# Performance work log

Measured on AMD Instinct MI355X. Metric: run time of the kernel, lower is better.

The kernel has to match this reference:

```python
import jax, jax.numpy as jnp
import numpy as np

NUM_HEADS = 8
NUM_GROUPS = 32
EPS = 1e-5


def group_norm(x, gamma, beta):
    b, c, h, w = x.shape
    xg = x.reshape(b, NUM_GROUPS, c // NUM_GROUPS, h, w)
    mean = jnp.mean(xg, axis=(2, 3, 4), keepdims=True)
    var = jnp.var(xg, axis=(2, 3, 4), keepdims=True)
    xn = ((xg - mean) * jax.lax.rsqrt(var + EPS)).reshape(b, c, h, w)
    return xn * gamma[None, :, None, None] + beta[None, :, None, None]


def setup_inputs() -> dict:
    key = jax.random.key(0)
    ks = jax.random.split(key, 4)
    b, c, h, w = 16, 512, 32, 32
    x = jax.random.normal(ks[0], (b, c, h, w), dtype=jnp.float32)
    gn_gamma = jnp.ones((c,), dtype=jnp.float32)
    gn_beta = jnp.zeros((c,), dtype=jnp.float32)
    qkv_w = jax.random.normal(ks[1], (3 * c, c), dtype=jnp.float32) * (1.0 / np.sqrt(c))
    qkv_b = jnp.zeros((3 * c,), dtype=jnp.float32)
    proj_w = jax.random.normal(ks[2], (c, c), dtype=jnp.float32) * (1.0 / np.sqrt(c))
    proj_b = jnp.zeros((c,), dtype=jnp.float32)
    return {"x": x, "gn_gamma": gn_gamma, "gn_beta": gn_beta,
            "qkv_w": qkv_w, "qkv_b": qkv_b, "proj_w": proj_w, "proj_b": proj_b}


def reference(x, gn_gamma, gn_beta, qkv_w, qkv_b, proj_w, proj_b):
    b, c, h, w = x.shape
    hd = c // NUM_HEADS
    hw = h * w

    xn = group_norm(x, gn_gamma, gn_beta)
    # 1x1 conv == channel matmul
    qkv = jnp.einsum('oc,bchw->bohw', qkv_w, xn) + qkv_b[None, :, None, None]
    q, k, v = jnp.split(qkv, 3, axis=1)
    q = q.reshape(b, NUM_HEADS, hd, hw)
    k = k.reshape(b, NUM_HEADS, hd, hw)
    v = v.reshape(b, NUM_HEADS, hd, hw)

    scale = 1.0 / np.sqrt(hd)
    attn = jnp.einsum('bhdt,bhds->bhts', q, k) * scale  # [b,H,hw,hw]
    attn = jax.nn.softmax(attn, axis=-1)
    h_attn = jnp.einsum('bhts,bhds->bhdt', attn, v).reshape(b, c, h, w)

    h_attn = jnp.einsum('oc,bchw->bohw', proj_w, h_attn) + proj_b[None, :, None, None]
    return x + h_attn
```

## Files before the change

### kernel.cpp

```cpp
#include <hip/hip_runtime.h>
#include <math.h>

#define NUM_HEADS 8
#define NUM_GROUPS 32
#define EPS 1e-5f

constexpr int B  = 16;
constexpr int C  = 512;
constexpr int HW = 1024;
constexpr int HD = 64;

typedef short bf16x8 __attribute__((ext_vector_type(8)));
typedef float f32x4  __attribute__((ext_vector_type(4)));

#define QSCALE 0.1803368801111f

__device__ inline unsigned short f2bf(float f) {
    union { float f; unsigned int u; } v; v.f = f;
    unsigned int r = (v.u + 0x7FFFu + ((v.u >> 16) & 1u)) >> 16;
    return (unsigned short)r;
}

__device__ __forceinline__ unsigned int pack_trunc(float lo, float hi) {
    return __builtin_amdgcn_perm(__float_as_uint(hi), __float_as_uint(lo), 0x07060302u);
}

__device__ __forceinline__ float exp2_raw(float x) {
#if __has_builtin(__builtin_amdgcn_exp2f)
    return __builtin_amdgcn_exp2f(x);
#else
    float r; asm("v_exp_f32 %0, %1" : "=v"(r) : "v"(x)); return r;
#endif
}

__device__ __forceinline__ void gld_lds16(void* lds, const void* g) {
    __builtin_amdgcn_global_load_lds(
        (const __attribute__((address_space(1))) void*)g,
        (__attribute__((address_space(3))) void*)lds, 16, 0, 0);
}

__device__ __forceinline__ void pl32_swap(unsigned int& a, unsigned int& b) {
#if __has_builtin(__builtin_amdgcn_permlane32_swap)
    auto r = __builtin_amdgcn_permlane32_swap(a, b, false, false);
    a = r[0]; b = r[1];
#else
    asm volatile("v_permlane32_swap_b32 %0, %1" : "+v"(a), "+v"(b));
#endif
}
__device__ __forceinline__ void pl16_swap(unsigned int& a, unsigned int& b) {
#if __has_builtin(__builtin_amdgcn_permlane16_swap)
    auto r = __builtin_amdgcn_permlane16_swap(a, b, false, false);
    a = r[0]; b = r[1];
#else
    asm volatile("v_permlane16_swap_b32 %0, %1" : "+v"(a), "+v"(b));
#endif
}

#define ABAR(VM) do {                                                   \
    asm volatile("s_waitcnt vmcnt(" VM ")\n\ts_barrier" ::: "memory");  \
    __builtin_amdgcn_sched_barrier(0);                                  \
} while (0)

__global__ __launch_bounds__(256)
void groupnorm_t_kernel(const float* __restrict__ x,
                        const float* __restrict__ gamma,
                        const float* __restrict__ beta,
                        unsigned short* __restrict__ xnT) {
    const int bg = blockIdx.x;
    const int b = bg >> 5, g = bg & 31;
    const size_t base = ((size_t)b * C + (size_t)g * 16) * HW;

    float v[4][16];
    float sum = 0.f, sumsq = 0.f;
    #pragma unroll
    for (int p = 0; p < 4; ++p) {
        const int t = threadIdx.x + p * 256;
        #pragma unroll
        for (int cl = 0; cl < 16; ++cl) {
            const float f = x[base + (size_t)cl * HW + t];
            v[p][cl] = f;
            sum += f;
            sumsq += f * f;
        }
    }
    #pragma unroll
    for (int off = 32; off > 0; off >>= 1) {
        sum   += __shfl_down(sum, off, 64);
        sumsq += __shfl_down(sumsq, off, 64);
    }
    __shared__ float s_sum[4], s_sq[4];
    const int wid = threadIdx.x >> 6, lane = threadIdx.x & 63;
    if (lane == 0) { s_sum[wid] = sum; s_sq[wid] = sumsq; }
    __syncthreads();
    const float tsum = s_sum[0] + s_sum[1] + s_sum[2] + s_sum[3];
    const float tsq  = s_sq[0] + s_sq[1] + s_sq[2] + s_sq[3];
    const float mean = tsum * (1.0f / 16384.f);
    const float var  = tsq * (1.0f / 16384.f) - mean * mean;
    const float rstd = rsqrtf(var + EPS);

    float ga[16], be[16];
    #pragma unroll
    for (int cl = 0; cl < 16; ++cl) {
        ga[cl] = gamma[g * 16 + cl] * rstd;
        be[cl] = beta[g * 16 + cl] - mean * ga[cl];
    }

    #pragma unroll
    for (int p = 0; p < 4; ++p) {
        const int t = threadIdx.x + p * 256;
        unsigned short pk[16];
        #pragma unroll
        for (int cl = 0; cl < 16; ++cl)
            pk[cl] = f2bf(v[p][cl] * ga[cl] + be[cl]);
        unsigned short* dst = xnT + ((size_t)(b * 1024 + t)) * 512 + g * 16;
        *(uint4*)dst = *(const uint4*)pk;
        *(uint4*)(dst + 8) = *(const uint4*)(pk + 8);
    }
}

__global__ __launch_bounds__(256)
void wconv_kernel(const float* __restrict__ qkv_w,
                  const float* __restrict__ proj_w,
                  unsigned short* __restrict__ wqb) {
    const int i = blockIdx.x * 256 + threadIdx.x;
    const int n1 = 786432 / 4;
    const int nt = 1048576 / 4;
    if (i >= nt) return;
    const float4 v = (i < n1) ? ((const float4*)qkv_w)[i]
                              : ((const float4*)proj_w)[i - n1];
    ushort4 r;
    r.x = f2bf(v.x); r.y = f2bf(v.y); r.z = f2bf(v.z); r.w = f2bf(v.w);
    ((ushort4*)wqb)[i] = r;
}

__device__ __forceinline__ void mfma_gemm_core(const char* __restrict__ Ab,
                                               const char* __restrict__ Bb,
                                               unsigned short* As,
                                               unsigned short* Bs,
                                               f32x4 acc[4][4]) {
    const int tid = threadIdx.x;
    const int w = tid >> 6, lane = tid & 63;
    const int lo = lane & 15, q4 = lane >> 4;
    const int wm = w >> 1, wn = w & 1;
    const int lrow = lane >> 2, lkc = lane & 3;

    for (int k0 = 0; k0 < 512; k0 += 32) {
        __syncthreads();
        #pragma unroll
        for (int i = 0; i < 2; ++i) {
            const int row = w * 32 + i * 16 + lrow;
            const int kc = lkc ^ ((row >> 1) & 3);
            const size_t goff = (size_t)row * 1024 + k0 * 2 + kc * 16;
            gld_lds16((char*)As + w * 2048 + i * 1024, Ab + goff);
            gld_lds16((char*)Bs + w * 2048 + i * 1024, Bb + goff);
        }
        __syncthreads();

        bf16x8 af[4], bfr[4];
        #pragma unroll
        for (int i = 0; i < 4; ++i) {
            const int ra = wm * 64 + i * 16 + lo;
            af[i]  = *(const bf16x8*)(As + ra * 32 + (q4 ^ ((ra >> 1) & 3)) * 8);
            const int rb = wn * 64 + i * 16 + lo;
            bfr[i] = *(const bf16x8*)(Bs + rb * 32 + (q4 ^ ((rb >> 1) & 3)) * 8);
        }
        #pragma unroll
        for (int mi = 0; mi < 4; ++mi)
            #pragma unroll
            for (int ni = 0; ni < 4; ++ni)
                acc[mi][ni] = __builtin_amdgcn_mfma_f32_16x16x32_bf16(
                    af[mi], bfr[ni], acc[mi][ni], 0, 0, 0);
    }
}

__global__ __launch_bounds__(256)
void qkv_mfma_kernel(const unsigned short* __restrict__ wqb,
                     const unsigned short* __restrict__ xnT,
                     const float* __restrict__ qkv_b,
                     unsigned short* __restrict__ Qt,
                     unsigned short* __restrict__ Kt,
                     unsigned short* __restrict__ Vb) {
    __shared__ __align__(16) unsigned short SMEM[8192];
    unsigned short* As = SMEM;
    unsigned short* Bs = SMEM + 4096;
    const int batch = blockIdx.z;
    const int mBase = blockIdx.y * 128, nBase = blockIdx.x * 128;

    f32x4 acc[4][4] = {};
    mfma_gemm_core((const char*)(wqb + (size_t)mBase * 512),
                   (const char*)(xnT + ((size_t)batch * 1024 + nBase) * 512),
                   As, Bs, acc);

    const int tid = threadIdx.x;
    const int w = tid >> 6, lane = tid & 63;
    const int lo = lane & 15, q4 = lane >> 4;
    const int wm = w >> 1, wn = w & 1;
    const int mw = mBase + wm * 64;
    const int tb = nBase + wn * 64;

    __syncthreads();

    if (mw < 1024) {
        const bool isQ = mw < 512;
        const int head = (mw >> 6) & 7;
        unsigned short* dst = (isQ ? Qt : Kt) + (((size_t)batch * 8 + head) << 16);
        const float sc = isQ ? QSCALE : 1.0f;
        #pragma unroll
        for (int mi = 0; mi < 4; ++mi) {
            const float4 bq = *(const float4*)(qkv_b + mw + mi * 16 + q4 * 4);
            #pragma unroll
            for (int ni = 0; ni < 4; ++ni) {
                const int t = tb + ni * 16 + lo;
                ushort4 pk;
                pk.x = f2bf((acc[mi][ni][0] + bq.x) * sc);
                pk.y = f2bf((acc[mi][ni][1] + bq.y) * sc);
                pk.z = f2bf((acc[mi][ni][2] + bq.z) * sc);
                pk.w = f2bf((acc[mi][ni][3] + bq.w) * sc);
                *(ushort4*)(dst + (size_t)t * 64 + mi * 16 + q4 * 4) = pk;
            }
        }
    } else {
        unsigned short* T = SMEM + w * 2048;
        unsigned short* Vrow = Vb + (size_t)batch * 524288 + (size_t)(mw - 1024) * 1024 + tb;
        const int rl8 = lane >> 3, c8 = lane & 7;
        #pragma unroll
        for (int p = 0; p < 2; ++p) {
            #pragma unroll
            for (int mi2 = 0; mi2 < 2; ++mi2) {
                const int mi = 2 * p + mi2;
                const float4 bq = *(const float4*)(qkv_b + mw + mi * 16 + q4 * 4);
                const int dl = mi2 * 16 + q4 * 4;
                #pragma unroll
                for (int ni = 0; ni < 4; ++ni) {
                    const int tl = ni * 16 + lo;
                    T[(dl + 0) * 64 + tl] = f2bf(acc[mi][ni][0] + bq.x);
                    T[(dl + 1) * 64 + tl] = f2bf(acc[mi][ni][1] + bq.y);
                    T[(dl + 2) * 64 + tl] = f2bf(acc[mi][ni][2] + bq.z);
                    T[(dl + 3) * 64 + tl] = f2bf(acc[mi][ni][3] + bq.w);
                }
            }
            #pragma unroll
            for (int i = 0; i < 4; ++i) {
                const int dl = i * 8 + rl8;
                const uint4 val = *(const uint4*)&T[dl * 64 + c8 * 8];
                *(uint4*)(Vrow + (size_t)(p * 32 + dl) * 1024 + c8 * 8) = val;
            }
        }
    }
}

__device__ __forceinline__ void attn_stage(const unsigned short* __restrict__ Kp,
                                           const unsigned short* __restrict__ Vp,
                                           int s0, unsigned short* Kd,
                                           unsigned short* Vd,
                                           int w, int rl, int p8) {
    #pragma unroll
    for (int cc = 0; cc < 2; ++cc) {
        const int r = 16 * w + 8 * cc + rl;
        const int jj = p8 ^ (r & 7);
        gld_lds16(Kd + (16 * w + 8 * cc) * 64, Kp + (size_t)(s0 + r) * 64 + jj * 8);
        gld_lds16(Vd + (16 * w + 8 * cc) * 64, Vp + (size_t)r * 1024 + s0 + jj * 8);
    }
}

__device__ __forceinline__ void attn_chunk(const unsigned short* __restrict__ Kc,
                                           const unsigned short* __restrict__ Vc,
                                           const bf16x8 (&qf)[2][2],
                                           f32x4 (&oacc)[4][2], float (&lrun)[2],
                                           int lo, int q4, int xr) {
    f32x4 sacc[4][2] = {};
    __builtin_amdgcn_s_setprio(1);
    #pragma unroll
    for (int mt = 0; mt < 4; ++mt) {
        const unsigned short* kr = Kc + (16 * mt + lo) * 64;
        const bf16x8 a0 = *(const bf16x8*)(kr + ((q4    ) ^ xr) * 8);
        const bf16x8 a1 = *(const bf16x8*)(kr + ((q4 + 4) ^ xr) * 8);
        #pragma unroll
        for (int nt = 0; nt < 2; ++nt) {
            sacc[mt][nt] = __builtin_amdgcn_mfma_f32_16x16x32_bf16(a0, qf[nt][0], sacc[mt][nt], 0, 0, 0);
            sacc[mt][nt] = __builtin_amdgcn_mfma_f32_16x16x32_bf16(a1, qf[nt][1], sacc[mt][nt], 0, 0, 0);
        }
    }
    __builtin_amdgcn_s_setprio(0);

    bf16x8 bp[2][2];
    #pragma unroll
    for (int nt = 0; nt < 2; ++nt) {
        unsigned int X[4][2];
        float ps = 0.f;
        #pragma unroll
        for (int mt = 0; mt < 4; ++mt) {
            const f32x4 s = sacc[mt][nt];
            const float p0 = exp2_raw(s[0]);
            const float p1 = exp2_raw(s[1]);
            const float p2 = exp2_raw(s[2]);
            const float p3 = exp2_raw(s[3]);
            ps += (p0 + p1) + (p2 + p3);
            X[mt][0] = pack_trunc(p0, p1);
            X[mt][1] = pack_trunc(p2, p3);
        }
        lrun[nt] += ps;
        #pragma unroll
        for (int h2 = 0; h2 < 2; ++h2) {
            unsigned int Y0, Y1, Y2, Y3;
            {
                unsigned int a = X[2 * h2][0], bb = X[2 * h2 + 1][0];
                pl32_swap(a, bb);
                pl16_swap(a, bb);
                Y0 = a; Y2 = bb;
            }
            {
                unsigned int a = X[2 * h2][1], bb = X[2 * h2 + 1][1];
                pl32_swap(a, bb);
                pl16_swap(a, bb);
                Y1 = a; Y3 = bb;
            }
            union { unsigned int u[4]; bf16x8 v; } cv;
            cv.u[0] = Y0; cv.u[1] = Y1; cv.u[2] = Y2; cv.u[3] = Y3;
            bp[nt][h2] = cv.v;
        }
    }

    __builtin_amdgcn_s_setprio(1);
    #pragma unroll
    for (int md = 0; md < 4; ++md) {
        const unsigned short* vr = Vc + (16 * md + lo) * 64;
        const bf16x8 v0 = *(const bf16x8*)(vr + ((q4    ) ^ xr) * 8);
        const bf16x8 v1 = *(const bf16x8*)(vr + ((q4 + 4) ^ xr) * 8);
        #pragma unroll
        for (int nt = 0; nt < 2; ++nt) {
            oacc[md][nt] = __builtin_amdgcn_mfma_f32_16x16x32_bf16(v0, bp[nt][0], oacc[md][nt], 0, 0, 0);
            oacc[md][nt] = __builtin_amdgcn_mfma_f32_16x16x32_bf16(v1, bp[nt][1], oacc[md][nt], 0, 0, 0);
        }
    }
    __builtin_amdgcn_s_setprio(0);
}

__global__ __launch_bounds__(256, 3)
void attn_mfma_kernel(const unsigned short* __restrict__ Qt,
                      const unsigned short* __restrict__ Kt,
                      const unsigned short* __restrict__ Vb,
                      unsigned short* __restrict__ attnT) {
    const int bh = blockIdx.x;
    const int b = bh >> 3, h = bh & 7;
    const int tBase = blockIdx.y * 128;
    const int tid = threadIdx.x;
    const int w = tid >> 6, lane = tid & 63;
    const int lo = lane & 15, q4 = lane >> 4;
    const int xr = lo & 7;

    __shared__ __align__(16) unsigned short Ks[3][64 * 64];
    __shared__ __align__(16) unsigned short Vs[3][64 * 64];

    const unsigned short* Kp = Kt + ((size_t)bh << 16);
    const unsigned short* Vp = Vb + ((size_t)b * 512 + h * 64) * 1024;

    bf16x8 qf[2][2];
    {
        const unsigned short* Qp = Qt + ((size_t)bh * 1024 + tBase + 32 * w) * 64;
        #pragma unroll
        for (int nt = 0; nt < 2; ++nt) {
            qf[nt][0] = *(const bf16x8*)(Qp + (size_t)(16 * nt + lo) * 64 + 8 * q4);
            qf[nt][1] = *(const bf16x8*)(Qp + (size_t)(16 * nt + lo) * 64 + 32 + 8 * q4);
        }
    }

    const int rl = lane >> 3, p8 = lane & 7;

    f32x4 oacc[4][2] = {};
    float lrun[2] = {0.f, 0.f};

    attn_stage(Kp, Vp, 0 * 64, Ks[0], Vs[0], w, rl, p8);
    attn_stage(Kp, Vp, 1 * 64, Ks[1], Vs[1], w, rl, p8);

    ABAR("4");
    attn_stage(Kp, Vp, 2 * 64, Ks[2], Vs[2], w, rl, p8);
    attn_chunk(Ks[0], Vs[0], qf, oacc, lrun, lo, q4, xr);

    #pragma unroll 1
    for (int ii = 0; ii < 4; ++ii) {
        const int i = 3 * ii + 1;
        ABAR("4");
        attn_stage(Kp, Vp, (i + 2) * 64, Ks[0], Vs[0], w, rl, p8);
        attn_chunk(Ks[1], Vs[1], qf, oacc, lrun, lo, q4, xr);
        ABAR("4");
        attn_stage(Kp, Vp, (i + 3) * 64, Ks[1], Vs[1], w, rl, p8);
        attn_chunk(Ks[2], Vs[2], qf, oacc, lrun, lo, q4, xr);
        ABAR("4");
        attn_stage(Kp, Vp, (i + 4) * 64, Ks[2], Vs[2], w, rl, p8);
        attn_chunk(Ks[0], Vs[0], qf, oacc, lrun, lo, q4, xr);
    }

    ABAR("4");
    attn_stage(Kp, Vp, 15 * 64, Ks[0], Vs[0], w, rl, p8);
    attn_chunk(Ks[1], Vs[1], qf, oacc, lrun, lo, q4, xr);
    ABAR("4");
    attn_chunk(Ks[2], Vs[2], qf, oacc, lrun, lo, q4, xr);
    ABAR("0");
    attn_chunk(Ks[0], Vs[0], qf, oacc, lrun, lo, q4, xr);

    #pragma unroll
    for (int nt = 0; nt < 2; ++nt) {
        float lt = lrun[nt];
        lt += __shfl_xor(lt, 16, 64);
        lt += __shfl_xor(lt, 32, 64);
        const float inv = 1.0f / lt;
        const int t = tBase + 32 * w + 16 * nt + lo;
        unsigned short* op = attnT + ((size_t)(b * 1024 + t)) * 512 + h * 64;
        #pragma unroll
        for (int md = 0; md < 4; ++md) {
            uint2 pk;
            pk.x = pack_trunc(oacc[md][nt][0] * inv, oacc[md][nt][1] * inv);
            pk.y = pack_trunc(oacc[md][nt][2] * inv, oacc[md][nt][3] * inv);
            *(uint2*)(op + 16 * md + 4 * q4) = pk;
        }
    }
}

__global__ __launch_bounds__(256)
void proj_mfma_kernel(const unsigned short* __restrict__ wpb,
                      const unsigned short* __restrict__ attnT,
                      const float* __restrict__ proj_b,
                      const float* __restrict__ x,
                      float* __restrict__ out) {
    __shared__ __align__(16) unsigned short As[128 * 32];
    __shared__ __align__(16) unsigned short Bs[128 * 32];
    const int batch = blockIdx.z;
    const int mBase = blockIdx.y * 128, nBase = blockIdx.x * 128;

    f32x4 acc[4][4] = {};
    mfma_gemm_core((const char*)(wpb + (size_t)mBase * 512),
                   (const char*)(attnT + ((size_t)batch * 1024 + nBase) * 512),
                   As, Bs, acc);

    const int tid = threadIdx.x;
    const int w = tid >> 6, lane = tid & 63;
    const int lo = lane & 15, q4 = lane >> 4;
    const int wm = w >> 1, wn = w & 1;
    const float* xb = x + (size_t)batch * 524288;
    float* ob = out + (size_t)batch * 524288;

    #pragma unroll
    for (int mi = 0; mi < 4; ++mi) {
        const int m0 = mBase + wm * 64 + mi * 16 + q4 * 4;
        const float4 bq = *(const float4*)(proj_b + m0);
        #pragma unroll
        for (int ni = 0; ni < 4; ++ni) {
            const int t = nBase + wn * 64 + ni * 16 + lo;
            const size_t o0 = (size_t)m0 * 1024 + t;
            ob[o0]          = acc[mi][ni][0] + bq.x + xb[o0];
            ob[o0 + 1024]   = acc[mi][ni][1] + bq.y + xb[o0 + 1024];
            ob[o0 + 2048]   = acc[mi][ni][2] + bq.z + xb[o0 + 2048];
            ob[o0 + 3072]   = acc[mi][ni][3] + bq.w + xb[o0 + 3072];
        }
    }
}

extern "C" void kernel_launch(void* const* d_in, const int* in_sizes, int n_in,
                              void* d_out, int out_size, void* d_ws, size_t ws_size,
                              hipStream_t stream) {
    const float* x        = (const float*)d_in[0];
    const float* gn_gamma = (const float*)d_in[1];
    const float* gn_beta  = (const float*)d_in[2];
    const float* qkv_w    = (const float*)d_in[3];
    const float* qkv_b    = (const float*)d_in[4];
    const float* proj_w   = (const float*)d_in[5];
    const float* proj_b   = (const float*)d_in[6];
    float* out = (float*)d_out;

    char* wsc = (char*)d_ws;
    unsigned short* xnT   = (unsigned short*)(wsc);
    unsigned short* Qt    = (unsigned short*)(wsc + 16777216);
    unsigned short* Kt    = (unsigned short*)(wsc + 33554432);
    unsigned short* Vb    = (unsigned short*)(wsc + 50331648);
    unsigned short* attnT = (unsigned short*)(wsc + 67108864);
    unsigned short* wqb   = (unsigned short*)(wsc + 83886080);
    unsigned short* wpb   = wqb + 786432;

    groupnorm_t_kernel<<<B * NUM_GROUPS, 256, 0, stream>>>(x, gn_gamma, gn_beta, xnT);

    wconv_kernel<<<1024, 256, 0, stream>>>(qkv_w, proj_w, wqb);

    {
        dim3 grid(HW / 128, (3 * C) / 128, B);
        qkv_mfma_kernel<<<grid, 256, 0, stream>>>(wqb, xnT, qkv_b, Qt, Kt, Vb);
    }

    {
        dim3 grid(B * NUM_HEADS, HW / 128);
        attn_mfma_kernel<<<grid, 256, 0, stream>>>(Qt, Kt, Vb, attnT);
    }

    {
        dim3 grid(HW / 128, C / 128, B);
        proj_mfma_kernel<<<grid, 256, 0, stream>>>(wpb, attnT, proj_b, x, out);
    }
}
```

Measured before the change: 212.7 us.

## Triple-buffer LDS in QKV and projection GEMMs with async load pipelining

Replaces the single-buffered K loop of the shared MFMA GEMM core with a three-stage LDS ring. Global-to-LDS loads for future K steps are issued while MFMAs run on the current stage, and waits use a partial ABAR macro instead of two full syncthreads per step. MFMA sections are also wrapped in s_setprio to favour matrix issue. LDS per block triples, which may lower occupancy, and correctness depends on the ABAR counts matching the outstanding loads.

```diff
diff --git a/kernel.cpp b/kernel.cpp
--- a/kernel.cpp
+++ b/kernel.cpp
@@ -133,10 +133,46 @@
     ((ushort4*)wqb)[i] = r;
 }
 
-__device__ __forceinline__ void mfma_gemm_core(const char* __restrict__ Ab,
+__device__ __forceinline__ void gemm_stage(const char* __restrict__ Ab,
+                                           const char* __restrict__ Bb,
+                                           int step, unsigned short* As,
+                                           unsigned short* Bs,
+                                           int w, int lrow, int lkc) {
+    #pragma unroll
+    for (int i = 0; i < 2; ++i) {
+        const int row = w * 32 + i * 16 + lrow;
+        const int kc = lkc ^ ((row >> 1) & 3);
+        const size_t goff = (size_t)row * 1024 + (size_t)step * 64 + kc * 16;
+        gld_lds16((char*)As + w * 2048 + i * 1024, Ab + goff);
+        gld_lds16((char*)Bs + w * 2048 + i * 1024, Bb + goff);
+    }
+}
+
+__device__ __forceinline__ void gemm_step(const unsigned short* __restrict__ As,
+                                          const unsigned short* __restrict__ Bs,
+                                          f32x4 acc[4][4],
+                                          int lo, int q4, int wm, int wn) {
+    bf16x8 af[4], bfr[4];
+    #pragma unroll
+    for (int i = 0; i < 4; ++i) {
+        const int ra = wm * 64 + i * 16 + lo;
+        af[i]  = *(const bf16x8*)(As + ra * 32 + (q4 ^ ((ra >> 1) & 3)) * 8);
+        const int rb = wn * 64 + i * 16 + lo;
+        bfr[i] = *(const bf16x8*)(Bs + rb * 32 + (q4 ^ ((rb >> 1) & 3)) * 8);
+    }
+    __builtin_amdgcn_s_setprio(1);
+    #pragma unroll
+    for (int mi = 0; mi < 4; ++mi)
+        #pragma unroll
+        for (int ni = 0; ni < 4; ++ni)
+            acc[mi][ni] = __builtin_amdgcn_mfma_f32_16x16x32_bf16(
+                af[mi], bfr[ni], acc[mi][ni], 0, 0, 0);
+    __builtin_amdgcn_s_setprio(0);
+}
+
+__device__ __forceinline__ void mfma_gemm_pipe(const char* __restrict__ Ab,
                                                const char* __restrict__ Bb,
-                                               unsigned short* As,
-                                               unsigned short* Bs,
+                                               unsigned short* S,
                                                f32x4 acc[4][4]) {
     const int tid = threadIdx.x;
     const int w = tid >> 6, lane = tid & 63;
@@ -144,33 +180,37 @@
     const int wm = w >> 1, wn = w & 1;
     const int lrow = lane >> 2, lkc = lane & 3;
 
-    for (int k0 = 0; k0 < 512; k0 += 32) {
-        __syncthreads();
-        #pragma unroll
-        for (int i = 0; i < 2; ++i) {
-            const int row = w * 32 + i * 16 + lrow;
-            const int kc = lkc ^ ((row >> 1) & 3);
-            const size_t goff = (size_t)row * 1024 + k0 * 2 + kc * 16;
-            gld_lds16((char*)As + w * 2048 + i * 1024, Ab + goff);
-            gld_lds16((char*)Bs + w * 2048 + i * 1024, Bb + goff);
-        }
-        __syncthreads();
-
-        bf16x8 af[4], bfr[4];
-        #pragma unroll
-        for (int i = 0; i < 4; ++i) {
-            const int ra = wm * 64 + i * 16 + lo;
-            af[i]  = *(const bf16x8*)(As + ra * 32 + (q4 ^ ((ra >> 1) & 3)) * 8);
-            const int rb = wn * 64 + i * 16 + lo;
-            bfr[i] = *(const bf16x8*)(Bs + rb * 32 + (q4 ^ ((rb >> 1) & 3)) * 8);
-        }
-        #pragma unroll
-        for (int mi = 0; mi < 4; ++mi)
-            #pragma unroll
-            for (int ni = 0; ni < 4; ++ni)
-                acc[mi][ni] = __builtin_amdgcn_mfma_f32_16x16x32_bf16(
-                    af[mi], bfr[ni], acc[mi][ni], 0, 0, 0);
-    }
+    unsigned short* A0 = S;             unsigned short* B0 = S + 4096;
+    unsigned short* A1 = S + 8192;      unsigned short* B1 = S + 12288;
+    unsigned short* A2 = S + 16384;     unsigned short* B2 = S + 20480;
+
+    gemm_stage(Ab, Bb, 0, A0, B0, w, lrow, lkc);
+    gemm_stage(Ab, Bb, 1, A1, B1, w, lrow, lkc);
+    ABAR("4");
+    gemm_stage(Ab, Bb, 2, A2, B2, w, lrow, lkc);
+    gemm_step(A0, B0, acc, lo, q4, wm, wn);
+
+    #pragma unroll 1
+    for (int ii = 0; ii < 4; ++ii) {
+        const int i = 3 * ii + 1;
+        ABAR("4");
+        gemm_stage(Ab, Bb, i + 2, A0, B0, w, lrow, lkc);
+        gemm_step(A1, B1, acc, lo, q4, wm, wn);
+        ABAR("4");
+        gemm_stage(Ab, Bb, i + 3, A1, B1, w, lrow, lkc);
+        gemm_step(A2, B2, acc, lo, q4, wm, wn);
+        ABAR("4");
+        gemm_stage(Ab, Bb, i + 4, A2, B2, w, lrow, lkc);
+        gemm_step(A0, B0, acc, lo, q4, wm, wn);
+    }
+
+    ABAR("4");
+    gemm_stage(Ab, Bb, 15, A0, B0, w, lrow, lkc);
+    gemm_step(A1, B1, acc, lo, q4, wm, wn);
+    ABAR("4");
+    gemm_step(A2, B2, acc, lo, q4, wm, wn);
+    ABAR("0");
+    gemm_step(A0, B0, acc, lo, q4, wm, wn);
 }
 
 __global__ __launch_bounds__(256)
@@ -180,16 +220,14 @@
                      unsigned short* __restrict__ Qt,
                      unsigned short* __restrict__ Kt,
                      unsigned short* __restrict__ Vb) {
-    __shared__ __align__(16) unsigned short SMEM[8192];
-    unsigned short* As = SMEM;
-    unsigned short* Bs = SMEM + 4096;
+    __shared__ __align__(16) unsigned short SMEM[3 * 8192];
     const int batch = blockIdx.z;
     const int mBase = blockIdx.y * 128, nBase = blockIdx.x * 128;
 
     f32x4 acc[4][4] = {};
-    mfma_gemm_core((const char*)(wqb + (size_t)mBase * 512),
+    mfma_gemm_pipe((const char*)(wqb + (size_t)mBase * 512),
                    (const char*)(xnT + ((size_t)batch * 1024 + nBase) * 512),
-                   As, Bs, acc);
+                   SMEM, acc);
 
     const int tid = threadIdx.x;
     const int w = tid >> 6, lane = tid & 63;
@@ -423,15 +461,14 @@
                       const float* __restrict__ proj_b,
                       const float* __restrict__ x,
                       float* __restrict__ out) {
-    __shared__ __align__(16) unsigned short As[128 * 32];
-    __shared__ __align__(16) unsigned short Bs[128 * 32];
+    __shared__ __align__(16) unsigned short SMEM[3 * 8192];
     const int batch = blockIdx.z;
     const int mBase = blockIdx.y * 128, nBase = blockIdx.x * 128;
 
     f32x4 acc[4][4] = {};
-    mfma_gemm_core((const char*)(wpb + (size_t)mBase * 512),
+    mfma_gemm_pipe((const char*)(wpb + (size_t)mBase * 512),
                    (const char*)(attnT + ((size_t)batch * 1024 + nBase) * 512),
-                   As, Bs, acc);
+                   SMEM, acc);
 
     const int tid = threadIdx.x;
     const int w = tid >> 6, lane = tid & 63;
```

After: 206.1 us. 3.1% less time.
